# Performance work log

Hardware: AMD Instinct MI355X
Metric: run time of the kernel (lower is better)

Reference implementation:

```python
import jax, jax.numpy as jnp
import numpy as np


def setup_inputs() -> dict:
    key = jax.random.key(0)
    k1, k2, k3 = jax.random.split(key, 3)
    B, D, L = 32768, 1024, 2
    return {
        "x": jax.random.normal(k1, (B, D), dtype=jnp.float32),
        "local_angles": jax.random.normal(k2, (L, D), dtype=jnp.float32),
        "ent_angles": jax.random.normal(k3, (L, D // 2), dtype=jnp.float32),
    }


def _local_layer(out, angles):
    # Sequential chain of Givens rotations on column pairs (i, (i+1)%D).
    # Each step uses the already-updated columns, exactly like the torch loop
    # (out = out @ R.T  ==  rotate columns i and j of out).
    D = out.shape[1]
    idx = jnp.arange(D)

    def body(o, inp):
        i, theta = inp
        j = (i + 1) % D
        c, s = jnp.cos(theta), jnp.sin(theta)
        ci = jnp.take(o, i, axis=1)  # [B]
        cj = jnp.take(o, j, axis=1)  # [B]
        o = o.at[:, i].set(c * ci - s * cj)
        o = o.at[:, j].set(s * ci + c * cj)
        return o, None

    out, _ = jax.lax.scan(body, out, (idx, angles))
    return out


def _ent_layer(out, angles):
    # Entangler rotations act on disjoint pairs (2k, 2k+1) -> fully vectorized.
    B, D = out.shape
    p = out.reshape(B, D // 2, 2)
    c, s = jnp.cos(angles), jnp.sin(angles)  # [D//2]
    x0, x1 = p[..., 0], p[..., 1]
    return jnp.stack([c * x0 - s * x1, s * x0 + c * x1], axis=-1).reshape(B, D)


def reference(x, local_angles, ent_angles):
    out = x
    num_layers = local_angles.shape[0]
    for l in range(num_layers):
        out = _local_layer(out, local_angles[l])
        out = _ent_layer(out, ent_angles[l])
    return out
```

## Files before the change

kernel.cpp:

```cpp
#include <hip/hip_runtime.h>

#define D_DIM    1024
#define PER_LANE 16
#define NLAYER   2
#define NPAIR    8
#define WPB      4

typedef float nf4 __attribute__((ext_vector_type(4)));

__device__ __forceinline__ int swz(int c) { return c ^ ((c >> 3) & 7); }

template<int CTRL, int RMASK>
__device__ __forceinline__ float dpp_mov(float src, float oldv) {
    return __int_as_float(__builtin_amdgcn_update_dpp(
        __float_as_int(oldv), __float_as_int(src), CTRL, RMASK, 0xF, false));
}

__global__ void angles_kernel(const float* __restrict__ la,
                              const float* __restrict__ ea,
                              float* __restrict__ tab) {
    int t  = blockIdx.x * blockDim.x + threadIdx.x;
    int nt = gridDim.x * blockDim.x;
    for (int i = t; i < NLAYER * D_DIM; i += nt) {
        float s, c; sincosf(la[i], &s, &c);
        tab[i] = c; tab[2048 + i] = s;
    }
    for (int i = t; i < NLAYER * (D_DIM / 2); i += nt) {
        float s, c; sincosf(ea[i], &s, &c);
        tab[4096 + i] = c; tab[5120 + i] = s;
    }
}

__global__ __launch_bounds__(256) void qent_kernel(
        const float* __restrict__ x,
        const float* __restrict__ tab,
        float* __restrict__ out, int B)
{
    const int lane  = threadIdx.x & 63;
    const int wid   = threadIdx.x >> 6;
    const int gwave = blockIdx.x * WPB + wid;
    const int nwave = gridDim.x * WPB;

    __shared__ float4 tb[WPB][2][256];
    __shared__ float2 lds_ces[NLAYER][NPAIR][64];

    for (int t = threadIdx.x; t < NLAYER * 512; t += 256) {
        int L = t >> 9, p = t & 511;
        int m = p >> 6, ln = p & 63;
        float2 cs;
        cs.x = tab[4096 + L * 512 + ln * 8 + m];
        cs.y = tab[5120 + L * 512 + ln * 8 + m];
        lds_ces[L][m][ln] = cs;
    }
    __syncthreads();

    float cl[NLAYER][PER_LANE], sl[NLAYER][PER_LANE];
    #pragma unroll
    for (int L = 0; L < NLAYER; ++L) {
        const float4* cp = reinterpret_cast<const float4*>(tab + L * D_DIM + lane * PER_LANE);
        const float4* sp = reinterpret_cast<const float4*>(tab + 2048 + L * D_DIM + lane * PER_LANE);
        #pragma unroll
        for (int q = 0; q < 4; ++q) {
            float4 c4 = cp[q], s4 = sp[q];
            cl[L][4*q+0] = c4.x; cl[L][4*q+1] = c4.y; cl[L][4*q+2] = c4.z; cl[L][4*q+3] = c4.w;
            sl[L][4*q+0] = s4.x; sl[L][4*q+1] = s4.y; sl[L][4*q+2] = s4.z; sl[L][4*q+3] = s4.w;
        }
    }

    const int l2 = lane ^ (lane >> 3);
    auto stage = [&](int b, int row) {
        const float* src = x + (size_t)row * D_DIM;
        #pragma unroll
        for (int q = 0; q < 4; ++q) {
            __builtin_amdgcn_global_load_lds(
                (const __attribute__((address_space(1))) void*)(src + q * 256 + l2 * 4),
                (__attribute__((address_space(3))) void*)&tb[wid][b][q * 64],
                16, 0, 0);
        }
    };

    stage(0, gwave);

    int it = 0;
    for (int row = gwave; row < B; row += nwave, ++it) {
        const int cur  = it & 1;
        const int nrow = row + nwave;

        if (nrow < B) {
            stage(cur ^ 1, nrow);
            if (it == 0) asm volatile("s_waitcnt vmcnt(4)" ::: "memory");
            else         asm volatile("s_waitcnt vmcnt(8)" ::: "memory");
        } else {
            asm volatile("s_waitcnt vmcnt(0)" ::: "memory");
        }

        float v[PER_LANE];
        #pragma unroll
        for (int r = 0; r < 4; ++r) {
            float4 t = tb[wid][cur][swz(4 * lane + r)];
            v[4*r+0] = t.x; v[4*r+1] = t.y; v[4*r+2] = t.z; v[4*r+3] = t.w;
        }

        #pragma unroll
        for (int L = 0; L < NLAYER; ++L) {
            float vnf = dpp_mov<0x130, 0xF>(v[0], v[0]);

            float A = 1.f, Bv = 0.f;
            #pragma unroll
            for (int k = 0; k < PER_LANE; ++k) {
                float vn = (k < PER_LANE - 1) ? v[k + 1] : vnf;
                Bv = sl[L][k] * Bv + cl[L][k] * vn;
                A  = sl[L][k] * A;
            }

            float Ai = A, Bi = Bv;
            #define SCAN_STEP(CTRL, RMASK) do {                   \
                float Au = dpp_mov<CTRL, RMASK>(Ai, 1.0f);        \
                float Bu = dpp_mov<CTRL, RMASK>(Bi, 0.0f);        \
                Bi = fmaf(Ai, Bu, Bi);                            \
                Ai *= Au; } while (0)
            SCAN_STEP(0x111, 0xF);
            SCAN_STEP(0x112, 0xF);
            SCAN_STEP(0x114, 0xF);
            SCAN_STEP(0x118, 0xF);
            SCAN_STEP(0x142, 0xA);
            SCAN_STEP(0x143, 0xC);
            #undef SCAN_STEP

            float Ax = dpp_mov<0x138, 0xF>(Ai, 0.0f);
            float Bx = dpp_mov<0x138, 0xF>(Bi, 0.0f);
            float v0b = __int_as_float(
                __builtin_amdgcn_readfirstlane(__float_as_int(v[0])));
            float u   = (lane == 0) ? v[0] : fmaf(Ax, v0b, Bx);

            #pragma unroll
            for (int k = 0; k < PER_LANE - 1; ++k) {
                float vn = v[k + 1];
                float f  = cl[L][k] * u - sl[L][k] * vn;
                u        = sl[L][k] * u + cl[L][k] * vn;
                v[k] = f;
            }
            float a0 = __int_as_float(
                __builtin_amdgcn_readfirstlane(__float_as_int(v[0])));
            float vn15 = (lane == 63) ? a0 : vnf;
            float f15  = cl[L][PER_LANE-1] * u - sl[L][PER_LANE-1] * vn15;
            float un   = sl[L][PER_LANE-1] * u + cl[L][PER_LANE-1] * vn15;
            v[PER_LANE-1] = f15;
            float f0new = __int_as_float(
                __builtin_amdgcn_readlane(__float_as_int(un), 63));
            v[0] = (lane == 0) ? f0new : v[0];

            #pragma unroll
            for (int m = 0; m < NPAIR; ++m) {
                float2 cs = lds_ces[L][m][lane];
                float x0 = v[2*m], x1 = v[2*m+1];
                v[2*m]   = cs.x * x0 - cs.y * x1;
                v[2*m+1] = cs.y * x0 + cs.x * x1;
            }
        }

        #pragma unroll
        for (int r = 0; r < 4; ++r) {
            float4 t;
            t.x = v[4*r+0]; t.y = v[4*r+1]; t.z = v[4*r+2]; t.w = v[4*r+3];
            tb[wid][cur][swz(4 * lane + r)] = t;
        }
        nf4* op = reinterpret_cast<nf4*>(out + (size_t)row * D_DIM);
        #pragma unroll
        for (int q = 0; q < 4; ++q) {
            float4 t = tb[wid][cur][swz(q * 64 + lane)];
            nf4 w; w.x = t.x; w.y = t.y; w.z = t.z; w.w = t.w;
            __builtin_nontemporal_store(w, &op[q * 64 + lane]);
        }
    }
}

extern "C" void kernel_launch(void* const* d_in, const int* in_sizes, int n_in,
                              void* d_out, int out_size, void* d_ws, size_t ws_size,
                              hipStream_t stream) {
    const float* x  = (const float*)d_in[0];
    const float* la = (const float*)d_in[1];
    const float* ea = (const float*)d_in[2];
    float* out = (float*)d_out;
    float* tab = (float*)d_ws;
    int B = in_sizes[0] / D_DIM;

    angles_kernel<<<64, 256, 0, stream>>>(la, ea, tab);
    qent_kernel<<<1024, 256, 0, stream>>>(x, tab, out, B);
}
```

Measured before the change: 54.71 us.

## Process two rows per iteration with contiguous per-wave row blocks

Each wave now handles a contiguous block of 16 rows, eight iterations of two rows each, instead of grid-striding one row at a time. Two rows are staged into LDS per prefetch, so more loads are in flight, and the grid is halved to 512 blocks. The loop count is hardcoded and no longer checks B, so it only works when B equals 512*4*16. LDS per block doubles, which may reduce occupancy, and the waitcnt accounting must match the extra stores between stages.

```diff
diff --git a/kernel.cpp b/kernel.cpp
--- a/kernel.cpp
+++ b/kernel.cpp
@@ -5,6 +5,9 @@
 #define NLAYER   2
 #define NPAIR    8
 #define WPB      4
+#define NITER    8
+#define ROWS_PI  2
+#define ROWS_PW  (NITER * ROWS_PI)
 
 typedef float nf4 __attribute__((ext_vector_type(4)));
 
@@ -39,9 +42,8 @@
     const int lane  = threadIdx.x & 63;
     const int wid   = threadIdx.x >> 6;
     const int gwave = blockIdx.x * WPB + wid;
-    const int nwave = gridDim.x * WPB;
-
-    __shared__ float4 tb[WPB][2][256];
+
+    __shared__ float4 tb[WPB][2][2 * 256];
     __shared__ float2 lds_ces[NLAYER][NPAIR][64];
 
     for (int t = threadIdx.x; t < NLAYER * 512; t += 256) {
@@ -68,109 +70,117 @@
     }
 
     const int l2 = lane ^ (lane >> 3);
-    auto stage = [&](int b, int row) {
-        const float* src = x + (size_t)row * D_DIM;
+    auto stage2 = [&](int b, int row) {
         #pragma unroll
-        for (int q = 0; q < 4; ++q) {
-            __builtin_amdgcn_global_load_lds(
-                (const __attribute__((address_space(1))) void*)(src + q * 256 + l2 * 4),
-                (__attribute__((address_space(3))) void*)&tb[wid][b][q * 64],
-                16, 0, 0);
+        for (int h = 0; h < ROWS_PI; ++h) {
+            const float* src = x + (size_t)(row + h) * D_DIM;
+            #pragma unroll
+            for (int q = 0; q < 4; ++q) {
+                __builtin_amdgcn_global_load_lds(
+                    (const __attribute__((address_space(1))) void*)(src + q * 256 + l2 * 4),
+                    (__attribute__((address_space(3))) void*)&tb[wid][b][h * 256 + q * 64],
+                    16, 0, 0);
+            }
         }
     };
 
-    stage(0, gwave);
-
-    int it = 0;
-    for (int row = gwave; row < B; row += nwave, ++it) {
+    const int row0 = gwave * ROWS_PW;
+    stage2(0, row0);
+
+    for (int it = 0; it < NITER; ++it) {
         const int cur  = it & 1;
-        const int nrow = row + nwave;
-
-        if (nrow < B) {
-            stage(cur ^ 1, nrow);
-            if (it == 0) asm volatile("s_waitcnt vmcnt(4)" ::: "memory");
-            else         asm volatile("s_waitcnt vmcnt(8)" ::: "memory");
+        const int rbase = row0 + it * ROWS_PI;
+
+        if (it + 1 < NITER) {
+            stage2(cur ^ 1, rbase + ROWS_PI);
+            if (it == 0) asm volatile("s_waitcnt vmcnt(8)"  ::: "memory");
+            else         asm volatile("s_waitcnt vmcnt(16)" ::: "memory");
         } else {
-            asm volatile("s_waitcnt vmcnt(0)" ::: "memory");
-        }
-
-        float v[PER_LANE];
+            asm volatile("s_waitcnt vmcnt(8)" ::: "memory");
+        }
+
         #pragma unroll
-        for (int r = 0; r < 4; ++r) {
-            float4 t = tb[wid][cur][swz(4 * lane + r)];
-            v[4*r+0] = t.x; v[4*r+1] = t.y; v[4*r+2] = t.z; v[4*r+3] = t.w;
-        }
-
-        #pragma unroll
-        for (int L = 0; L < NLAYER; ++L) {
-            float vnf = dpp_mov<0x130, 0xF>(v[0], v[0]);
-
-            float A = 1.f, Bv = 0.f;
-            #pragma unroll
-            for (int k = 0; k < PER_LANE; ++k) {
-                float vn = (k < PER_LANE - 1) ? v[k + 1] : vnf;
-                Bv = sl[L][k] * Bv + cl[L][k] * vn;
-                A  = sl[L][k] * A;
-            }
-
-            float Ai = A, Bi = Bv;
-            #define SCAN_STEP(CTRL, RMASK) do {                   \
-                float Au = dpp_mov<CTRL, RMASK>(Ai, 1.0f);        \
-                float Bu = dpp_mov<CTRL, RMASK>(Bi, 0.0f);        \
-                Bi = fmaf(Ai, Bu, Bi);                            \
-                Ai *= Au; } while (0)
-            SCAN_STEP(0x111, 0xF);
-            SCAN_STEP(0x112, 0xF);
-            SCAN_STEP(0x114, 0xF);
-            SCAN_STEP(0x118, 0xF);
-            SCAN_STEP(0x142, 0xA);
-            SCAN_STEP(0x143, 0xC);
-            #undef SCAN_STEP
-
-            float Ax = dpp_mov<0x138, 0xF>(Ai, 0.0f);
-            float Bx = dpp_mov<0x138, 0xF>(Bi, 0.0f);
-            float v0b = __int_as_float(
-                __builtin_amdgcn_readfirstlane(__float_as_int(v[0])));
-            float u   = (lane == 0) ? v[0] : fmaf(Ax, v0b, Bx);
-
-            #pragma unroll
-            for (int k = 0; k < PER_LANE - 1; ++k) {
-                float vn = v[k + 1];
-                float f  = cl[L][k] * u - sl[L][k] * vn;
-                u        = sl[L][k] * u + cl[L][k] * vn;
-                v[k] = f;
-            }
-            float a0 = __int_as_float(
-                __builtin_amdgcn_readfirstlane(__float_as_int(v[0])));
-            float vn15 = (lane == 63) ? a0 : vnf;
-            float f15  = cl[L][PER_LANE-1] * u - sl[L][PER_LANE-1] * vn15;
-            float un   = sl[L][PER_LANE-1] * u + cl[L][PER_LANE-1] * vn15;
-            v[PER_LANE-1] = f15;
-            float f0new = __int_as_float(
-                __builtin_amdgcn_readlane(__float_as_int(un), 63));
-            v[0] = (lane == 0) ? f0new : v[0];
-
-            #pragma unroll
-            for (int m = 0; m < NPAIR; ++m) {
-                float2 cs = lds_ces[L][m][lane];
-                float x0 = v[2*m], x1 = v[2*m+1];
-                v[2*m]   = cs.x * x0 - cs.y * x1;
-                v[2*m+1] = cs.y * x0 + cs.x * x1;
-            }
-        }
-
-        #pragma unroll
-        for (int r = 0; r < 4; ++r) {
-            float4 t;
-            t.x = v[4*r+0]; t.y = v[4*r+1]; t.z = v[4*r+2]; t.w = v[4*r+3];
-            tb[wid][cur][swz(4 * lane + r)] = t;
-        }
-        nf4* op = reinterpret_cast<nf4*>(out + (size_t)row * D_DIM);
-        #pragma unroll
-        for (int q = 0; q < 4; ++q) {
-            float4 t = tb[wid][cur][swz(q * 64 + lane)];
-            nf4 w; w.x = t.x; w.y = t.y; w.z = t.z; w.w = t.w;
-            __builtin_nontemporal_store(w, &op[q * 64 + lane]);
+        for (int h = 0; h < ROWS_PI; ++h) {
+            const int hb = h * 256;
+
+            float v[PER_LANE];
+            #pragma unroll
+            for (int r = 0; r < 4; ++r) {
+                float4 t = tb[wid][cur][hb + swz(4 * lane + r)];
+                v[4*r+0] = t.x; v[4*r+1] = t.y; v[4*r+2] = t.z; v[4*r+3] = t.w;
+            }
+
+            #pragma unroll
+            for (int L = 0; L < NLAYER; ++L) {
+                float vnf = dpp_mov<0x130, 0xF>(v[0], v[0]);
+
+                float A = 1.f, Bv = 0.f;
+                #pragma unroll
+                for (int k = 0; k < PER_LANE; ++k) {
+                    float vn = (k < PER_LANE - 1) ? v[k + 1] : vnf;
+                    Bv = sl[L][k] * Bv + cl[L][k] * vn;
+                    A  = sl[L][k] * A;
+                }
+
+                float Ai = A, Bi = Bv;
+                #define SCAN_STEP(CTRL, RMASK) do {                   \
+                    float Au = dpp_mov<CTRL, RMASK>(Ai, 1.0f);        \
+                    float Bu = dpp_mov<CTRL, RMASK>(Bi, 0.0f);        \
+                    Bi = fmaf(Ai, Bu, Bi);                            \
+                    Ai *= Au; } while (0)
+                SCAN_STEP(0x111, 0xF);
+                SCAN_STEP(0x112, 0xF);
+                SCAN_STEP(0x114, 0xF);
+                SCAN_STEP(0x118, 0xF);
+                SCAN_STEP(0x142, 0xA);
+                SCAN_STEP(0x143, 0xC);
+                #undef SCAN_STEP
+
+                float Ax = dpp_mov<0x138, 0xF>(Ai, 0.0f);
+                float Bx = dpp_mov<0x138, 0xF>(Bi, 0.0f);
+                float v0b = __int_as_float(
+                    __builtin_amdgcn_readfirstlane(__float_as_int(v[0])));
+                float u   = (lane == 0) ? v[0] : fmaf(Ax, v0b, Bx);
+
+                #pragma unroll
+                for (int k = 0; k < PER_LANE - 1; ++k) {
+                    float vn = v[k + 1];
+                    float f  = cl[L][k] * u - sl[L][k] * vn;
+                    u        = sl[L][k] * u + cl[L][k] * vn;
+                    v[k] = f;
+                }
+                float a0 = __int_as_float(
+                    __builtin_amdgcn_readfirstlane(__float_as_int(v[0])));
+                float vn15 = (lane == 63) ? a0 : vnf;
+                float f15  = cl[L][PER_LANE-1] * u - sl[L][PER_LANE-1] * vn15;
+                float un   = sl[L][PER_LANE-1] * u + cl[L][PER_LANE-1] * vn15;
+                v[PER_LANE-1] = f15;
+                float f0new = __int_as_float(
+                    __builtin_amdgcn_readlane(__float_as_int(un), 63));
+                v[0] = (lane == 0) ? f0new : v[0];
+
+                #pragma unroll
+                for (int m = 0; m < NPAIR; ++m) {
+                    float2 cs = lds_ces[L][m][lane];
+                    float x0 = v[2*m], x1 = v[2*m+1];
+                    v[2*m]   = cs.x * x0 - cs.y * x1;
+                    v[2*m+1] = cs.y * x0 + cs.x * x1;
+                }
+            }
+
+            #pragma unroll
+            for (int r = 0; r < 4; ++r) {
+                float4 t;
+                t.x = v[4*r+0]; t.y = v[4*r+1]; t.z = v[4*r+2]; t.w = v[4*r+3];
+                tb[wid][cur][hb + swz(4 * lane + r)] = t;
+            }
+            nf4* op = reinterpret_cast<nf4*>(out + (size_t)(rbase + h) * D_DIM);
+            #pragma unroll
+            for (int q = 0; q < 4; ++q) {
+                float4 t = tb[wid][cur][hb + swz(q * 64 + lane)];
+                nf4 w; w.x = t.x; w.y = t.y; w.z = t.z; w.w = t.w;
+                __builtin_nontemporal_store(w, &op[q * 64 + lane]);
+            }
         }
     }
 }
@@ -186,5 +196,5 @@
     int B = in_sizes[0] / D_DIM;
 
     angles_kernel<<<64, 256, 0, stream>>>(la, ea, tab);
-    qent_kernel<<<1024, 256, 0, stream>>>(x, tab, out, B);
-}
+    qent_kernel<<<512, 256, 0, stream>>>(x, tab, out, B);
+}
```

New measurement: 55.25 us. No clear change (+1.0%).
